# Kernel tuning notes

Measured on AMD Instinct MI355X. Metric: run time of the kernel, lower is better.

## Reference

```python
import jax, jax.numpy as jnp
import numpy as np

DIM = 1024
INTER = 1024
E = 8            # n_routed_experts
TOP_K = 2        # n_activated_experts
ROUTE_SCALE = 1.0
B, S = 2, 1024


def setup_inputs() -> dict:
    key = jax.random.key(0)
    ks = jax.random.split(key, 8)
    scale = 0.02
    x = jax.random.normal(ks[0], (B, S, DIM), dtype=jnp.float32)
    gate_w = jax.random.normal(ks[1], (DIM, E), dtype=jnp.float32) * scale
    w1 = jax.random.normal(ks[2], (E, DIM, INTER), dtype=jnp.float32) * scale
    w2 = jax.random.normal(ks[3], (E, INTER, DIM), dtype=jnp.float32) * scale
    w3 = jax.random.normal(ks[4], (E, DIM, INTER), dtype=jnp.float32) * scale
    sw1 = jax.random.normal(ks[5], (DIM, INTER), dtype=jnp.float32) * scale
    sw2 = jax.random.normal(ks[6], (INTER, DIM), dtype=jnp.float32) * scale
    sw3 = jax.random.normal(ks[7], (DIM, INTER), dtype=jnp.float32) * scale
    return {"x": x, "gate_w": gate_w, "w1": w1, "w2": w2, "w3": w3,
            "sw1": sw1, "sw2": sw2, "sw3": sw3}


def reference(x, gate_w, w1, w2, w3, sw1, sw2, sw3):
    b, s, d = x.shape
    xt = x.reshape(-1, d)                      # [T, D]
    T = xt.shape[0]

    # --- TokenChoiceTopKRouter (score_func='softmax') ---
    scores = jax.nn.softmax((xt @ gate_w).astype(jnp.float32), axis=-1)  # [T, E]
    top_scores, top_idx = jax.lax.top_k(scores, TOP_K)                   # [T, K]
    top_scores = top_scores * ROUTE_SCALE

    # Dense combine weights [T, E]: scatter top-k routing weights per token.
    cw = jnp.zeros((T, E), dtype=xt.dtype)
    cw = cw.at[jnp.arange(T)[:, None], top_idx].set(top_scores.astype(xt.dtype))

    # --- GroupedExperts: SwiGLU per routed expert ---
    h1 = jnp.einsum('td,edh->teh', xt, w1)     # [T, E, INTER]
    h3 = jnp.einsum('td,edh->teh', xt, w3)
    h = jax.nn.silu(h1) * h3
    expert_out = jnp.einsum('teh,ehd->ted', h, w2)   # [T, E, D]

    # Combine: weighted sum over activated experts (zero weight elsewhere).
    routed = jnp.einsum('ted,te->td', expert_out, cw)

    # --- Shared expert (runs on all tokens) ---
    shared = (jax.nn.silu(xt @ sw1) * (xt @ sw3)) @ sw2

    return (routed + shared).reshape(b, s, d)
```

## Files before the change

kernel.cpp:

```cpp
#include <hip/hip_runtime.h>
#include <hip/hip_bf16.h>
#include <cstdint>
#include <cstddef>

#define DIM   1024
#define INTER 1024
#define NT    2048

typedef __attribute__((ext_vector_type(4))) float  f32x4;
typedef __attribute__((ext_vector_type(8))) short  s16x8;
typedef __attribute__((ext_vector_type(8))) unsigned short u16x8;

#define WS_CNT    0u
#define WS_SLOT   256u
#define WS_ASSIGN 33024u
#define WS_WT     65792u
#define WS_WTS2   98560u
#define WS_XB     131584u
#define WS_H      4325888u
#define WS_W1T    16908800u
#define WS_W3T    33686016u
#define WS_W2T    50463232u
#define WS_SW1T   67240448u
#define WS_SW3T   69337600u
#define WS_SW2T   71434752u
#define WS_NEED   73531904u
#define WS_OBUF   WS_W1T

__device__ __forceinline__ unsigned short f2bf(float f) {
    unsigned int u = __float_as_uint(f);
    return (unsigned short)((u + 0x7fffu + ((u >> 16) & 1u)) >> 16);
}
__device__ __forceinline__ float bf2f(unsigned short v) {
    return __uint_as_float(((unsigned int)v) << 16);
}

__device__ __forceinline__ void cp16(const void* g, void* l) {
    __builtin_amdgcn_global_load_lds((const __attribute__((address_space(1))) void*)g,
                                     (__attribute__((address_space(3))) void*)l, 16, 0, 0);
}

__global__ __launch_bounds__(256) void kfat1(
    const float* __restrict__ x, const float* __restrict__ gw,
    const float* __restrict__ w1, const float* __restrict__ w3,
    const float* __restrict__ sw1, const float* __restrict__ sw3,
    unsigned short* __restrict__ w1t, unsigned short* __restrict__ w3t,
    unsigned short* __restrict__ sw1t, unsigned short* __restrict__ sw3t,
    int* __restrict__ assign, float2* __restrict__ wts2, unsigned short* __restrict__ xb)
{
    __shared__ __align__(16) char smem[65536];
    int bid = blockIdx.x;
    int tid = threadIdx.x;
    if (bid < 1152) {
        int slab = bid >> 6, t = bid & 63;
        int r0 = (t >> 3) * 128, c0 = (t & 7) * 128;
        const float* src; unsigned short* dst;
        if (slab < 8)        { src = w1 + (size_t)slab * DIM * INTER;       dst = w1t + (size_t)slab * DIM * INTER; }
        else if (slab < 16)  { src = w3 + (size_t)(slab - 8) * DIM * INTER; dst = w3t + (size_t)(slab - 8) * DIM * INTER; }
        else if (slab == 16) { src = sw1; dst = sw1t; }
        else                 { src = sw3; dst = sw3t; }

        char* buf0 = smem;
        char* buf1 = smem + 32768;
        int w = tid >> 6, l = tid & 63;
        size_t lanoff = (size_t)(l >> 5) * 4096 + (size_t)(l & 31) * 16;
        const char* gbase = (const char*)src + (size_t)r0 * 4096 + (size_t)c0 * 4;

        #pragma unroll
        for (int i = 0; i < 8; ++i)
            cp16(gbase + (size_t)(w * 16 + i * 2) * 4096 + lanoff, buf0 + (w * 16 + i * 2) * 512);
        #pragma unroll
        for (int i = 0; i < 8; ++i)
            cp16(gbase + (size_t)(64 + w * 16 + i * 2) * 4096 + lanoff, buf1 + (w * 16 + i * 2) * 512);

        asm volatile("s_waitcnt vmcnt(8)" ::: "memory");
        __builtin_amdgcn_sched_barrier(0);
        __builtin_amdgcn_s_barrier();
        __builtin_amdgcn_sched_barrier(0);
        {
            const float* ldsf = (const float*)buf0;
            #pragma unroll
            for (int i = 0; i < 4; ++i) {
                int f = w * 4 + i;
                int ntl = f >> 1, ktl = f & 1;
                u16x8 o;
                #pragma unroll
                for (int j = 0; j < 8; ++j)
                    o[j] = f2bf(ldsf[(ktl * 32 + (l >> 4) * 8 + j) * 128 + ntl * 16 + (l & 15)]);
                size_t off = ((size_t)((c0 >> 4) + ntl) * 32 + (r0 >> 5) + ktl) * 512 + l * 8;
                *(u16x8*)(dst + off) = o;
            }
        }
        asm volatile("s_waitcnt vmcnt(0)" ::: "memory");
        __builtin_amdgcn_sched_barrier(0);
        __builtin_amdgcn_s_barrier();
        __builtin_amdgcn_sched_barrier(0);
        {
            const float* ldsf = (const float*)buf1;
            #pragma unroll
            for (int i = 0; i < 4; ++i) {
                int f = w * 4 + i;
                int ntl = f >> 1, ktl = f & 1;
                u16x8 o;
                #pragma unroll
                for (int j = 0; j < 8; ++j)
                    o[j] = f2bf(ldsf[(ktl * 32 + (l >> 4) * 8 + j) * 128 + ntl * 16 + (l & 15)]);
                size_t off = ((size_t)((c0 >> 4) + ntl) * 32 + (r0 >> 5) + 2 + ktl) * 512 + l * 8;
                *(u16x8*)(dst + off) = o;
            }
        }
        return;
    }
    int wid = tid >> 6, lane = tid & 63;
    int t = (bid - 1152) * 4 + wid;
    const float* xrow = x + (size_t)t * DIM;

    float xr[16];
    float acc[8] = {0.f,0.f,0.f,0.f,0.f,0.f,0.f,0.f};
    #pragma unroll
    for (int j = 0; j < 16; ++j) {
        float xv = xrow[j * 64 + lane];
        xr[j] = xv;
        const f32x4* g = (const f32x4*)(gw + (size_t)(j * 64 + lane) * 8);
        f32x4 g0 = g[0], g1 = g[1];
        acc[0] += xv * g0[0]; acc[1] += xv * g0[1]; acc[2] += xv * g0[2]; acc[3] += xv * g0[3];
        acc[4] += xv * g1[0]; acc[5] += xv * g1[1]; acc[6] += xv * g1[2]; acc[7] += xv * g1[3];
    }
    #pragma unroll
    for (int j = 0; j < 16; ++j) xb[(size_t)t * DIM + j * 64 + lane] = f2bf(xr[j]);

    #pragma unroll
    for (int e = 0; e < 8; ++e) {
        float v = acc[e];
        v += __shfl_xor(v, 1);  v += __shfl_xor(v, 2);  v += __shfl_xor(v, 4);
        v += __shfl_xor(v, 8);  v += __shfl_xor(v, 16); v += __shfl_xor(v, 32);
        acc[e] = v;
    }
    float mx = acc[0];
    #pragma unroll
    for (int e = 1; e < 8; ++e) mx = fmaxf(mx, acc[e]);
    float p[8]; float se = 0.f;
    #pragma unroll
    for (int e = 0; e < 8; ++e) { p[e] = expf(acc[e] - mx); se += p[e]; }
    float inv = 1.0f / se;
    int i0 = 0; float b0 = p[0];
    #pragma unroll
    for (int e = 1; e < 8; ++e) if (p[e] > b0) { b0 = p[e]; i0 = e; }
    int i1 = -1; float b1 = -1.f;
    #pragma unroll
    for (int e = 0; e < 8; ++e) if (e != i0 && p[e] > b1) { b1 = p[e]; i1 = e; }
    if (lane == 0) {
        assign[t] = i0 | (i1 << 8);
        wts2[t] = make_float2(b0 * inv, b1 * inv);
    }
}

__global__ __launch_bounds__(256) void kscatter(const int* __restrict__ assign,
                                                const float2* __restrict__ wts2,
                                                int* __restrict__ cnt,
                                                int* __restrict__ slots,
                                                float* __restrict__ wts)
{
    __shared__ int h[8], pos[8];
    int tid = threadIdx.x, lane = tid & 63;
    if (tid < 8) h[tid] = 0;
    __syncthreads();

    for (int base = 0; base < NT; base += 256) {
        int a = assign[base + tid];
        int e0 = a & 255, e1 = (a >> 8) & 255;
        #pragma unroll
        for (int e = 0; e < 8; ++e) {
            unsigned long long m0 = __ballot(e0 == e);
            unsigned long long m1 = __ballot(e1 == e);
            if (lane == 0) {
                int c = __popcll(m0) + __popcll(m1);
                if (c) atomicAdd(&h[e], c);
            }
        }
    }
    __syncthreads();
    if (tid == 0) {
        int run = 0;
        #pragma unroll
        for (int e = 0; e < 8; ++e) {
            cnt[8 + e] = run; pos[e] = run;
            cnt[e] = h[e]; run += h[e];
        }
        cnt[16] = run;
    }
    __syncthreads();

    for (int base = 0; base < NT; base += 256) {
        int t = base + tid;
        int a = assign[t];
        float2 w = wts2[t];
        int e0 = a & 255, e1 = (a >> 8) & 255;
        unsigned long long lt = (1ull << lane) - 1ull;
        #pragma unroll
        for (int e = 0; e < 8; ++e) {
            unsigned long long m0 = __ballot(e0 == e);
            unsigned long long m1 = __ballot(e1 == e);
            int c = __popcll(m0) + __popcll(m1);
            int b = 0;
            if (lane == 0 && c) b = atomicAdd(&pos[e], c);
            b = __shfl(b, 0);
            if (e0 == e) { int r = __popcll(m0 & lt);                 slots[b + r] = t * 2;     wts[b + r] = w.x; }
            if (e1 == e) { int r = __popcll(m0) + __popcll(m1 & lt);  slots[b + r] = t * 2 + 1; wts[b + r] = w.y; }
        }
    }
}

__global__ __launch_bounds__(256) void kfat2(
    const unsigned short* __restrict__ xb,
    const unsigned short* __restrict__ w1t, const unsigned short* __restrict__ w3t,
    const unsigned short* __restrict__ sw1t, const unsigned short* __restrict__ sw3t,
    const int* __restrict__ cnt, const int* __restrict__ slots,
    unsigned short* __restrict__ hbuf,
    const float* __restrict__ w2, const float* __restrict__ sw2,
    unsigned short* __restrict__ w2t, unsigned short* __restrict__ sw2t)
{
    __shared__ __align__(16) char smem[34048];
    int z = blockIdx.z;
    int tid = threadIdx.x;
    if (z >= 9) {
        if (blockIdx.x >= 8) return;
        int slab = z - 9;
        const float* src; unsigned short* dst;
        if (slab < 8) { src = w2 + (size_t)slab * DIM * INTER; dst = w2t + (size_t)slab * DIM * INTER; }
        else          { src = sw2; dst = sw2t; }
        int r0 = blockIdx.y * 64, c0 = blockIdx.x * 128;

        int w = tid >> 6, l = tid & 63;
        size_t lanoff = (size_t)(l >> 5) * 4096 + (size_t)(l & 31) * 16;
        const char* gbase = (const char*)src + (size_t)r0 * 4096 + (size_t)c0 * 4;
        #pragma unroll
        for (int i = 0; i < 8; ++i)
            cp16(gbase + (size_t)(w * 16 + i * 2) * 4096 + lanoff, smem + (w * 16 + i * 2) * 512);
        asm volatile("s_waitcnt vmcnt(0)" ::: "memory");
        __builtin_amdgcn_sched_barrier(0);
        __builtin_amdgcn_s_barrier();
        __builtin_amdgcn_sched_barrier(0);
        const float* ldsf = (const float*)smem;
        #pragma unroll
        for (int i = 0; i < 4; ++i) {
            int f = w * 4 + i;
            int ntl = f >> 1, ktl = f & 1;
            u16x8 o;
            #pragma unroll
            for (int j = 0; j < 8; ++j)
                o[j] = f2bf(ldsf[(ktl * 32 + (l >> 4) * 8 + j) * 128 + ntl * 16 + (l & 15)]);
            size_t off = ((size_t)((c0 >> 4) + ntl) * 32 + (r0 >> 5) + ktl) * 512 + l * 8;
            *(u16x8*)(dst + off) = o;
        }
        return;
    }

    int e = z;
    int m0 = blockIdx.y * 128;
    int n0 = blockIdx.x * 64;
    int n_rows, lbase;
    if (e < 8) { n_rows = cnt[e]; lbase = cnt[8 + e]; } else { n_rows = NT; lbase = 0; }
    if (m0 >= n_rows) return;
    int rm = min(128, n_rows - m0);

    const unsigned short* b1p = (e < 8) ? (w1t + (size_t)e * DIM * INTER) : sw1t;
    const unsigned short* b3p = (e < 8) ? (w3t + (size_t)e * DIM * INTER) : sw3t;

    char* sA = smem;
    int* rowTok  = (int*)(smem + 32768);
    int* rowSlot = (int*)(smem + 33280);

    if (tid < 128) {
        int r = m0 + min(tid, rm - 1);
        int slot, tok;
        if (e < 8) { slot = slots[lbase + r]; tok = slot >> 1; }
        else       { tok = r; slot = 4096 + r; }
        rowTok[tid] = tok;
        rowSlot[tid] = slot;
    }
    __syncthreads();

    int wid = tid >> 6, lane = tid & 63;
    int wr = wid >> 1, wc = wid & 1;
    int swz_st = (((lane & 7) ^ (lane >> 3)) - (lane & 7)) * 16;

    const char* pA[4];
    #pragma unroll
    for (int q = 0; q < 4; ++q) {
        int row = (q * 4 + wid) * 8 + (lane >> 3);
        pA[q] = (const char*)(xb + (size_t)rowTok[row] * DIM) + (lane & 7) * 16 + swz_st;
    }
    const char* pB1[2]; const char* pB3[2];
    #pragma unroll
    for (int n = 0; n < 2; ++n) {
        int nt = (n0 >> 4) + wc * 2 + n;
        pB1[n] = (const char*)b1p + (size_t)nt * 32768 + lane * 16;
        pB3[n] = (const char*)b3p + (size_t)nt * 32768 + lane * 16;
    }

    int loA[2];
    #pragma unroll
    for (int ks = 0; ks < 2; ++ks) {
        int ch = ((ks * 4) + (lane >> 4)) ^ (lane & 7);
        loA[ks] = (wr * 64 + (lane & 15)) * 128 + ch * 16;
    }

    f32x4 acc1[4][2], acc3[4][2];
    #pragma unroll
    for (int m = 0; m < 4; ++m)
        #pragma unroll
        for (int n = 0; n < 2; ++n) { acc1[m][n] = (f32x4){0.f,0.f,0.f,0.f}; acc3[m][n] = (f32x4){0.f,0.f,0.f,0.f}; }

    s16x8 br1[2][2][2], br3[2][2][2];

    #pragma unroll
    for (int q = 0; q < 4; ++q) { cp16(pA[q], sA + (q * 4 + wid) * 1024); pA[q] += 128; }
    #pragma unroll
    for (int n = 0; n < 2; ++n)
        #pragma unroll
        for (int ks = 0; ks < 2; ++ks) {
            br1[0][n][ks] = *(const s16x8*)(pB1[n] + ks * 1024);
            br3[0][n][ks] = *(const s16x8*)(pB3[n] + ks * 1024);
        }

    for (int tt = 0; tt < 8; ++tt) {
        #pragma unroll
        for (int half = 0; half < 2; ++half) {
            if (half == 0 || tt < 7) {
                #pragma unroll
                for (int q = 0; q < 4; ++q) {
                    cp16(pA[q], sA + (half ^ 1) * 16384 + (q * 4 + wid) * 1024);
                    pA[q] += 128;
                }
                #pragma unroll
                for (int n = 0; n < 2; ++n)
                    #pragma unroll
                    for (int ks = 0; ks < 2; ++ks) {
                        br1[half ^ 1][n][ks] = *(const s16x8*)(pB1[n] + (half * 2 + 2 + ks) * 1024);
                        br3[half ^ 1][n][ks] = *(const s16x8*)(pB3[n] + (half * 2 + 2 + ks) * 1024);
                    }
                asm volatile("s_waitcnt vmcnt(12)" ::: "memory");
            } else {
                asm volatile("s_waitcnt vmcnt(0)" ::: "memory");
            }
            __builtin_amdgcn_sched_barrier(0);
            __builtin_amdgcn_s_barrier();
            __builtin_amdgcn_sched_barrier(0);

            #pragma unroll
            for (int ks = 0; ks < 2; ++ks) {
                s16x8 a[4];
                #pragma unroll
                for (int m = 0; m < 4; ++m)
                    a[m] = *(const s16x8*)(sA + half * 16384 + m * 2048 + loA[ks]);
                #pragma unroll
                for (int n = 0; n < 2; ++n) {
                    #pragma unroll
                    for (int m = 0; m < 4; ++m) {
                        acc1[m][n] = __builtin_amdgcn_mfma_f32_16x16x32_bf16(a[m], br1[half][n][ks], acc1[m][n], 0, 0, 0);
                        acc3[m][n] = __builtin_amdgcn_mfma_f32_16x16x32_bf16(a[m], br3[half][n][ks], acc3[m][n], 0, 0, 0);
                    }
                }
            }
            __builtin_amdgcn_sched_barrier(0);
            __builtin_amdgcn_s_barrier();
            __builtin_amdgcn_sched_barrier(0);
        }
        #pragma unroll
        for (int n = 0; n < 2; ++n) { pB1[n] += 4096; pB3[n] += 4096; }
    }

    #pragma unroll
    for (int m = 0; m < 4; ++m) {
        int rbase = wr * 64 + m * 16 + (lane >> 4) * 4;
        #pragma unroll
        for (int r = 0; r < 4; ++r) {
            int row = rbase + r;
            if (row < rm) {
                int hrow = rowSlot[row];
                #pragma unroll
                for (int n = 0; n < 2; ++n) {
                    float v1 = acc1[m][n][r], v3 = acc3[m][n][r];
                    float hv = (v1 / (1.0f + __expf(-v1))) * v3;
                    int col = n0 + wc * 32 + n * 16 + (lane & 15);
                    hbuf[(size_t)hrow * INTER + col] = f2bf(hv);
                }
            }
        }
    }
}

__global__ __launch_bounds__(256) void kgemm2(
    const unsigned short* __restrict__ hbuf,
    const unsigned short* __restrict__ w2t, const unsigned short* __restrict__ sw2t,
    const int* __restrict__ cnt, const int* __restrict__ slots,
    unsigned short* __restrict__ obuf)
{
    int e = blockIdx.z;
    int m0 = blockIdx.y * 128;
    int n0 = blockIdx.x * 64;
    int n_rows, lbase;
    if (e < 8) { n_rows = cnt[e]; lbase = cnt[8 + e]; } else { n_rows = NT; lbase = 0; }
    if (m0 >= n_rows) return;
    int rm = min(128, n_rows - m0);
    const unsigned short* bp = (e < 8) ? (w2t + (size_t)e * DIM * INTER) : sw2t;

    __shared__ __align__(16) char sA[2][16384];
    __shared__ int rowH[128];

    int tid = threadIdx.x;
    if (tid < 128) {
        int r = m0 + min(tid, rm - 1);
        rowH[tid] = (e < 8) ? slots[lbase + r] : (4096 + r);
    }
    __syncthreads();

    int wid = tid >> 6, lane = tid & 63;
    int wr = wid >> 1, wc = wid & 1;
    int swz_st = (((lane & 7) ^ (lane >> 3)) - (lane & 7)) * 16;

    const char* pA[4];
    #pragma unroll
    for (int q = 0; q < 4; ++q) {
        int row = (q * 4 + wid) * 8 + (lane >> 3);
        pA[q] = (const char*)(hbuf + (size_t)rowH[row] * INTER) + (lane & 7) * 16 + swz_st;
    }
    const char* pB[2];
    #pragma unroll
    for (int n = 0; n < 2; ++n) {
        int nt = (n0 >> 4) + wc * 2 + n;
        pB[n] = (const char*)bp + (size_t)nt * 32768 + lane * 16;
    }

    int loA[2];
    #pragma unroll
    for (int ks = 0; ks < 2; ++ks) {
        int ch = ((ks * 4) + (lane >> 4)) ^ (lane & 7);
        loA[ks] = (wr * 64 + (lane & 15)) * 128 + ch * 16;
    }

    f32x4 acc[4][2];
    #pragma unroll
    for (int m = 0; m < 4; ++m)
        #pragma unroll
        for (int n = 0; n < 2; ++n) acc[m][n] = (f32x4){0.f,0.f,0.f,0.f};

    s16x8 br[2][2][2];

    #pragma unroll
    for (int q = 0; q < 4; ++q) { cp16(pA[q], (char*)sA + (q * 4 + wid) * 1024); pA[q] += 128; }
    #pragma unroll
    for (int n = 0; n < 2; ++n)
        #pragma unroll
        for (int ks = 0; ks < 2; ++ks)
            br[0][n][ks] = *(const s16x8*)(pB[n] + ks * 1024);

    for (int tt = 0; tt < 8; ++tt) {
        #pragma unroll
        for (int half = 0; half < 2; ++half) {
            if (half == 0 || tt < 7) {
                #pragma unroll
                for (int q = 0; q < 4; ++q) {
                    cp16(pA[q], (char*)sA + (half ^ 1) * 16384 + (q * 4 + wid) * 1024);
                    pA[q] += 128;
                }
                #pragma unroll
                for (int n = 0; n < 2; ++n)
                    #pragma unroll
                    for (int ks = 0; ks < 2; ++ks)
                        br[half ^ 1][n][ks] = *(const s16x8*)(pB[n] + (half * 2 + 2 + ks) * 1024);
                asm volatile("s_waitcnt vmcnt(8)" ::: "memory");
            } else {
                asm volatile("s_waitcnt vmcnt(0)" ::: "memory");
            }
            __builtin_amdgcn_sched_barrier(0);
            __builtin_amdgcn_s_barrier();
            __builtin_amdgcn_sched_barrier(0);

            #pragma unroll
            for (int ks = 0; ks < 2; ++ks) {
                s16x8 a[4];
                #pragma unroll
                for (int m = 0; m < 4; ++m)
                    a[m] = *(const s16x8*)((const char*)sA + half * 16384 + m * 2048 + loA[ks]);
                #pragma unroll
                for (int n = 0; n < 2; ++n)
                    #pragma unroll
                    for (int m = 0; m < 4; ++m)
                        acc[m][n] = __builtin_amdgcn_mfma_f32_16x16x32_bf16(a[m], br[half][n][ks], acc[m][n], 0, 0, 0);
            }
            __builtin_amdgcn_sched_barrier(0);
            __builtin_amdgcn_s_barrier();
            __builtin_amdgcn_sched_barrier(0);
        }
        #pragma unroll
        for (int n = 0; n < 2; ++n) pB[n] += 4096;
    }

    #pragma unroll
    for (int m = 0; m < 4; ++m) {
        int rbase = wr * 64 + m * 16 + (lane >> 4) * 4;
        #pragma unroll
        for (int r = 0; r < 4; ++r) {
            int row = rbase + r;
            if (row < rm) {
                int orow = rowH[row];
                #pragma unroll
                for (int n = 0; n < 2; ++n) {
                    int col = n0 + wc * 32 + n * 16 + (lane & 15);
                    obuf[(size_t)orow * DIM + col] = f2bf(acc[m][n][r]);
                }
            }
        }
    }
}

__global__ __launch_bounds__(256) void kcombine(const unsigned short* __restrict__ obuf,
                                                const float2* __restrict__ wts2,
                                                float* __restrict__ out)
{
    int gid = blockIdx.x * 256 + threadIdx.x;
    int t = gid >> 7;
    int d0 = (gid & 127) * 8;
    float2 w = wts2[t];
    u16x8 r0 = *(const u16x8*)&obuf[(size_t)(2 * t)     * DIM + d0];
    u16x8 r1 = *(const u16x8*)&obuf[(size_t)(2 * t + 1) * DIM + d0];
    u16x8 rs = *(const u16x8*)&obuf[(size_t)(4096 + t)  * DIM + d0];
    f32x4 o0, o1;
    #pragma unroll
    for (int j = 0; j < 4; ++j) o0[j] = w.x * bf2f(r0[j]) + w.y * bf2f(r1[j]) + bf2f(rs[j]);
    #pragma unroll
    for (int j = 0; j < 4; ++j) o1[j] = w.x * bf2f(r0[4+j]) + w.y * bf2f(r1[4+j]) + bf2f(rs[4+j]);
    f32x4* dst = (f32x4*)&out[(size_t)t * DIM + d0];
    dst[0] = o0; dst[1] = o1;
}

extern "C" void kernel_launch(void* const* d_in, const int* in_sizes, int n_in,
                              void* d_out, int out_size, void* d_ws, size_t ws_size,
                              hipStream_t stream) {
    const float* x      = (const float*)d_in[0];
    const float* gate_w = (const float*)d_in[1];
    const float* w1     = (const float*)d_in[2];
    const float* w2     = (const float*)d_in[3];
    const float* w3     = (const float*)d_in[4];
    const float* sw1    = (const float*)d_in[5];
    const float* sw2    = (const float*)d_in[6];
    const float* sw3    = (const float*)d_in[7];
    float* out = (float*)d_out;

    if (ws_size < (size_t)WS_NEED) return;

    char* ws = (char*)d_ws;
    int*            cnt      = (int*)(ws + WS_CNT);
    int*            slots    = (int*)(ws + WS_SLOT);
    int*            assign   = (int*)(ws + WS_ASSIGN);
    float*          wts      = (float*)(ws + WS_WT);
    float2*         wts2     = (float2*)(ws + WS_WTS2);
    unsigned short* xb       = (unsigned short*)(ws + WS_XB);
    unsigned short* hbuf     = (unsigned short*)(ws + WS_H);
    unsigned short* w1t      = (unsigned short*)(ws + WS_W1T);
    unsigned short* w3t      = (unsigned short*)(ws + WS_W3T);
    unsigned short* w2t      = (unsigned short*)(ws + WS_W2T);
    unsigned short* sw1t     = (unsigned short*)(ws + WS_SW1T);
    unsigned short* sw3t     = (unsigned short*)(ws + WS_SW3T);
    unsigned short* sw2t     = (unsigned short*)(ws + WS_SW2T);
    unsigned short* obuf     = (unsigned short*)(ws + WS_OBUF);

    kfat1<<<dim3(1664), 256, 0, stream>>>(x, gate_w, w1, w3, sw1, sw3,
                                          w1t, w3t, sw1t, sw3t, assign, wts2, xb);
    kscatter<<<dim3(1), 256, 0, stream>>>(assign, wts2, cnt, slots, wts);
    kfat2<<<dim3(16, 16, 18), 256, 0, stream>>>(xb, w1t, w3t, sw1t, sw3t, cnt, slots, hbuf,
                                                w2, sw2, w2t, sw2t);
    kgemm2<<<dim3(16, 16, 9), 256, 0, stream>>>(hbuf, w2t, sw2t, cnt, slots, obuf);
    kcombine<<<dim3(1024), 256, 0, stream>>>(obuf, wts2, out);
}
```

Baseline: 133.4 us.

## Widen GEMM tiles to 128 columns with 512-thread blocks; split weight conversion finer

The grouped GEMM kernels (kfat2, kgemm2) now use 128x128 output tiles computed by 8 waves in 512-thread blocks instead of 128x64 tiles with 4 waves. Each wave now issues fewer A-tile async copies, and the vmcnt waits are adjusted to match. This halves the number of blocks and the redundant A-tile loads per output column, but lowers the block count available to fill the GPU. The weight-transpose/convert work in kfat1 is split into 64-row tiles without double buffering, doubling its block count and halving its LDS use. The w2 conversion inside kfat2 is also spread across all x-blocks, so none of them idle.

```diff
diff --git a/kernel.cpp b/kernel.cpp
--- a/kernel.cpp
+++ b/kernel.cpp
@@ -48,71 +48,44 @@
     unsigned short* __restrict__ sw1t, unsigned short* __restrict__ sw3t,
     int* __restrict__ assign, float2* __restrict__ wts2, unsigned short* __restrict__ xb)
 {
-    __shared__ __align__(16) char smem[65536];
+    __shared__ __align__(16) char smem[32768];
     int bid = blockIdx.x;
     int tid = threadIdx.x;
-    if (bid < 1152) {
-        int slab = bid >> 6, t = bid & 63;
-        int r0 = (t >> 3) * 128, c0 = (t & 7) * 128;
+    if (bid < 2304) {
+        int slab = bid >> 7, t = bid & 127;
+        int r0 = (t >> 3) * 64, c0 = (t & 7) * 128;
         const float* src; unsigned short* dst;
         if (slab < 8)        { src = w1 + (size_t)slab * DIM * INTER;       dst = w1t + (size_t)slab * DIM * INTER; }
         else if (slab < 16)  { src = w3 + (size_t)(slab - 8) * DIM * INTER; dst = w3t + (size_t)(slab - 8) * DIM * INTER; }
         else if (slab == 16) { src = sw1; dst = sw1t; }
         else                 { src = sw3; dst = sw3t; }
 
-        char* buf0 = smem;
-        char* buf1 = smem + 32768;
         int w = tid >> 6, l = tid & 63;
         size_t lanoff = (size_t)(l >> 5) * 4096 + (size_t)(l & 31) * 16;
         const char* gbase = (const char*)src + (size_t)r0 * 4096 + (size_t)c0 * 4;
-
         #pragma unroll
         for (int i = 0; i < 8; ++i)
-            cp16(gbase + (size_t)(w * 16 + i * 2) * 4096 + lanoff, buf0 + (w * 16 + i * 2) * 512);
-        #pragma unroll
-        for (int i = 0; i < 8; ++i)
-            cp16(gbase + (size_t)(64 + w * 16 + i * 2) * 4096 + lanoff, buf1 + (w * 16 + i * 2) * 512);
-
-        asm volatile("s_waitcnt vmcnt(8)" ::: "memory");
-        __builtin_amdgcn_sched_barrier(0);
-        __builtin_amdgcn_s_barrier();
-        __builtin_amdgcn_sched_barrier(0);
-        {
-            const float* ldsf = (const float*)buf0;
-            #pragma unroll
-            for (int i = 0; i < 4; ++i) {
-                int f = w * 4 + i;
-                int ntl = f >> 1, ktl = f & 1;
-                u16x8 o;
-                #pragma unroll
-                for (int j = 0; j < 8; ++j)
-                    o[j] = f2bf(ldsf[(ktl * 32 + (l >> 4) * 8 + j) * 128 + ntl * 16 + (l & 15)]);
-                size_t off = ((size_t)((c0 >> 4) + ntl) * 32 + (r0 >> 5) + ktl) * 512 + l * 8;
-                *(u16x8*)(dst + off) = o;
-            }
-        }
+            cp16(gbase + (size_t)(w * 16 + i * 2) * 4096 + lanoff, smem + (w * 16 + i * 2) * 512);
         asm volatile("s_waitcnt vmcnt(0)" ::: "memory");
         __builtin_amdgcn_sched_barrier(0);
         __builtin_amdgcn_s_barrier();
         __builtin_amdgcn_sched_barrier(0);
-        {
-            const float* ldsf = (const float*)buf1;
+        const float* ldsf = (const float*)smem;
+        #pragma unroll
+        for (int i = 0; i < 4; ++i) {
+            int f = w * 4 + i;
+            int ntl = f >> 1, ktl = f & 1;
+            u16x8 o;
             #pragma unroll
-            for (int i = 0; i < 4; ++i) {
-                int f = w * 4 + i;
-                int ntl = f >> 1, ktl = f & 1;
-                u16x8 o;
-                #pragma unroll
-                for (int j = 0; j < 8; ++j)
-                    o[j] = f2bf(ldsf[(ktl * 32 + (l >> 4) * 8 + j) * 128 + ntl * 16 + (l & 15)]);
-                size_t off = ((size_t)((c0 >> 4) + ntl) * 32 + (r0 >> 5) + 2 + ktl) * 512 + l * 8;
-                *(u16x8*)(dst + off) = o;
-            }
+            for (int j = 0; j < 8; ++j)
+                o[j] = f2bf(ldsf[(ktl * 32 + (l >> 4) * 8 + j) * 128 + ntl * 16 + (l & 15)]);
+            size_t off = ((size_t)((c0 >> 4) + ntl) * 32 + (r0 >> 5) + ktl) * 512 + l * 8;
+            *(u16x8*)(dst + off) = o;
         }
         return;
     }
     int wid = tid >> 6, lane = tid & 63;
-    int t = (bid - 1152) * 4 + wid;
+    int t = (bid - 2304) * 4 + wid;
     const float* xrow = x + (size_t)t * DIM;
 
     float xr[16];
@@ -211,7 +184,7 @@
     }
 }
 
-__global__ __launch_bounds__(256) void kfat2(
+__global__ __launch_bounds__(512) void kfat2(
     const unsigned short* __restrict__ xb,
     const unsigned short* __restrict__ w1t, const unsigned short* __restrict__ w3t,
     const unsigned short* __restrict__ sw1t, const unsigned short* __restrict__ sw3t,
@@ -220,11 +193,10 @@
     const float* __restrict__ w2, const float* __restrict__ sw2,
     unsigned short* __restrict__ w2t, unsigned short* __restrict__ sw2t)
 {
-    __shared__ __align__(16) char smem[34048];
+    __shared__ __align__(16) char smem[33792];
     int z = blockIdx.z;
     int tid = threadIdx.x;
     if (z >= 9) {
-        if (blockIdx.x >= 8) return;
         int slab = z - 9;
         const float* src; unsigned short* dst;
         if (slab < 8) { src = w2 + (size_t)slab * DIM * INTER; dst = w2t + (size_t)slab * DIM * INTER; }
@@ -235,16 +207,16 @@
         size_t lanoff = (size_t)(l >> 5) * 4096 + (size_t)(l & 31) * 16;
         const char* gbase = (const char*)src + (size_t)r0 * 4096 + (size_t)c0 * 4;
         #pragma unroll
-        for (int i = 0; i < 8; ++i)
-            cp16(gbase + (size_t)(w * 16 + i * 2) * 4096 + lanoff, smem + (w * 16 + i * 2) * 512);
+        for (int i = 0; i < 4; ++i)
+            cp16(gbase + (size_t)(w * 8 + i * 2) * 4096 + lanoff, smem + (w * 8 + i * 2) * 512);
         asm volatile("s_waitcnt vmcnt(0)" ::: "memory");
         __builtin_amdgcn_sched_barrier(0);
         __builtin_amdgcn_s_barrier();
         __builtin_amdgcn_sched_barrier(0);
         const float* ldsf = (const float*)smem;
         #pragma unroll
-        for (int i = 0; i < 4; ++i) {
-            int f = w * 4 + i;
+        for (int i = 0; i < 2; ++i) {
+            int f = w * 2 + i;
             int ntl = f >> 1, ktl = f & 1;
             u16x8 o;
             #pragma unroll
@@ -258,7 +230,7 @@
 
     int e = z;
     int m0 = blockIdx.y * 128;
-    int n0 = blockIdx.x * 64;
+    int n0 = blockIdx.x * 128;
     int n_rows, lbase;
     if (e < 8) { n_rows = cnt[e]; lbase = cnt[8 + e]; } else { n_rows = NT; lbase = 0; }
     if (m0 >= n_rows) return;
@@ -282,13 +254,13 @@
     __syncthreads();
 
     int wid = tid >> 6, lane = tid & 63;
-    int wr = wid >> 1, wc = wid & 1;
+    int wr = wid >> 2, wc = wid & 3;
     int swz_st = (((lane & 7) ^ (lane >> 3)) - (lane & 7)) * 16;
 
-    const char* pA[4];
-    #pragma unroll
-    for (int q = 0; q < 4; ++q) {
-        int row = (q * 4 + wid) * 8 + (lane >> 3);
+    const char* pA[2];
+    #pragma unroll
+    for (int q = 0; q < 2; ++q) {
+        int row = (q * 8 + wid) * 8 + (lane >> 3);
         pA[q] = (const char*)(xb + (size_t)rowTok[row] * DIM) + (lane & 7) * 16 + swz_st;
     }
     const char* pB1[2]; const char* pB3[2];
@@ -315,7 +287,7 @@
     s16x8 br1[2][2][2], br3[2][2][2];
 
     #pragma unroll
-    for (int q = 0; q < 4; ++q) { cp16(pA[q], sA + (q * 4 + wid) * 1024); pA[q] += 128; }
+    for (int q = 0; q < 2; ++q) { cp16(pA[q], sA + (q * 8 + wid) * 1024); pA[q] += 128; }
     #pragma unroll
     for (int n = 0; n < 2; ++n)
         #pragma unroll
@@ -329,8 +301,8 @@
         for (int half = 0; half < 2; ++half) {
             if (half == 0 || tt < 7) {
                 #pragma unroll
-                for (int q = 0; q < 4; ++q) {
-                    cp16(pA[q], sA + (half ^ 1) * 16384 + (q * 4 + wid) * 1024);
+                for (int q = 0; q < 2; ++q) {
+                    cp16(pA[q], sA + (half ^ 1) * 16384 + (q * 8 + wid) * 1024);
                     pA[q] += 128;
                 }
                 #pragma unroll
@@ -340,7 +312,7 @@
                         br1[half ^ 1][n][ks] = *(const s16x8*)(pB1[n] + (half * 2 + 2 + ks) * 1024);
                         br3[half ^ 1][n][ks] = *(const s16x8*)(pB3[n] + (half * 2 + 2 + ks) * 1024);
                     }
-                asm volatile("s_waitcnt vmcnt(12)" ::: "memory");
+                asm volatile("s_waitcnt vmcnt(10)" ::: "memory");
             } else {
                 asm volatile("s_waitcnt vmcnt(0)" ::: "memory");
             }
@@ -391,7 +363,7 @@
     }
 }
 
-__global__ __launch_bounds__(256) void kgemm2(
+__global__ __launch_bounds__(512) void kgemm2(
     const unsigned short* __restrict__ hbuf,
     const unsigned short* __restrict__ w2t, const unsigned short* __restrict__ sw2t,
     const int* __restrict__ cnt, const int* __restrict__ slots,
@@ -399,7 +371,7 @@
 {
     int e = blockIdx.z;
     int m0 = blockIdx.y * 128;
-    int n0 = blockIdx.x * 64;
+    int n0 = blockIdx.x * 128;
     int n_rows, lbase;
     if (e < 8) { n_rows = cnt[e]; lbase = cnt[8 + e]; } else { n_rows = NT; lbase = 0; }
     if (m0 >= n_rows) return;
@@ -417,13 +389,13 @@
     __syncthreads();
 
     int wid = tid >> 6, lane = tid & 63;
-    int wr = wid >> 1, wc = wid & 1;
+    int wr = wid >> 2, wc = wid & 3;
     int swz_st = (((lane & 7) ^ (lane >> 3)) - (lane & 7)) * 16;
 
-    const char* pA[4];
-    #pragma unroll
-    for (int q = 0; q < 4; ++q) {
-        int row = (q * 4 + wid) * 8 + (lane >> 3);
+    const char* pA[2];
+    #pragma unroll
+    for (int q = 0; q < 2; ++q) {
+        int row = (q * 8 + wid) * 8 + (lane >> 3);
         pA[q] = (const char*)(hbuf + (size_t)rowH[row] * INTER) + (lane & 7) * 16 + swz_st;
     }
     const char* pB[2];
@@ -449,7 +421,7 @@
     s16x8 br[2][2][2];
 
     #pragma unroll
-    for (int q = 0; q < 4; ++q) { cp16(pA[q], (char*)sA + (q * 4 + wid) * 1024); pA[q] += 128; }
+    for (int q = 0; q < 2; ++q) { cp16(pA[q], (char*)sA + (q * 8 + wid) * 1024); pA[q] += 128; }
     #pragma unroll
     for (int n = 0; n < 2; ++n)
         #pragma unroll
@@ -461,8 +433,8 @@
         for (int half = 0; half < 2; ++half) {
             if (half == 0 || tt < 7) {
                 #pragma unroll
-                for (int q = 0; q < 4; ++q) {
-                    cp16(pA[q], (char*)sA + (half ^ 1) * 16384 + (q * 4 + wid) * 1024);
+                for (int q = 0; q < 2; ++q) {
+                    cp16(pA[q], (char*)sA + (half ^ 1) * 16384 + (q * 8 + wid) * 1024);
                     pA[q] += 128;
                 }
                 #pragma unroll
@@ -470,7 +442,7 @@
                     #pragma unroll
                     for (int ks = 0; ks < 2; ++ks)
                         br[half ^ 1][n][ks] = *(const s16x8*)(pB[n] + (half * 2 + 2 + ks) * 1024);
-                asm volatile("s_waitcnt vmcnt(8)" ::: "memory");
+                asm volatile("s_waitcnt vmcnt(6)" ::: "memory");
             } else {
                 asm volatile("s_waitcnt vmcnt(0)" ::: "memory");
             }
@@ -567,11 +539,11 @@
     unsigned short* sw2t     = (unsigned short*)(ws + WS_SW2T);
     unsigned short* obuf     = (unsigned short*)(ws + WS_OBUF);
 
-    kfat1<<<dim3(1664), 256, 0, stream>>>(x, gate_w, w1, w3, sw1, sw3,
+    kfat1<<<dim3(2816), 256, 0, stream>>>(x, gate_w, w1, w3, sw1, sw3,
                                           w1t, w3t, sw1t, sw3t, assign, wts2, xb);
     kscatter<<<dim3(1), 256, 0, stream>>>(assign, wts2, cnt, slots, wts);
-    kfat2<<<dim3(16, 16, 18), 256, 0, stream>>>(xb, w1t, w3t, sw1t, sw3t, cnt, slots, hbuf,
-                                                w2, sw2, w2t, sw2t);
-    kgemm2<<<dim3(16, 16, 9), 256, 0, stream>>>(hbuf, w2t, sw2t, cnt, slots, obuf);
+    kfat2<<<dim3(8, 16, 18), 512, 0, stream>>>(xb, w1t, w3t, sw1t, sw3t, cnt, slots, hbuf,
+                                               w2, sw2, w2t, sw2t);
+    kgemm2<<<dim3(8, 16, 9), 512, 0, stream>>>(hbuf, w2t, sw2t, cnt, slots, obuf);
     kcombine<<<dim3(1024), 256, 0, stream>>>(obuf, wts2, out);
 }
```

New measurement: 145.4 us. 9.1% more time.

## Split weight-convert tiles and move B-register prefetch after MFMA compute

Applied to the files above, without the earlier changes.

The weight conversion blocks in kfat1 now each handle a 64x128 tile with a single 32KB LDS buffer instead of two 64-row halves in 64KB. This doubles the block count and cuts LDS per block, which should raise occupancy. In both GEMM kernels the main loop is peeled so that B-fragment register loads for the next stage are issued after the current MFMAs rather than before the wait. That gives global loads more time in flight, but it adds duplicated epilogue code and extra barriers.

```diff
diff --git a/kernel.cpp b/kernel.cpp
--- a/kernel.cpp
+++ b/kernel.cpp
@@ -48,71 +48,44 @@
     unsigned short* __restrict__ sw1t, unsigned short* __restrict__ sw3t,
     int* __restrict__ assign, float2* __restrict__ wts2, unsigned short* __restrict__ xb)
 {
-    __shared__ __align__(16) char smem[65536];
+    __shared__ __align__(16) char smem[32768];
     int bid = blockIdx.x;
     int tid = threadIdx.x;
-    if (bid < 1152) {
-        int slab = bid >> 6, t = bid & 63;
-        int r0 = (t >> 3) * 128, c0 = (t & 7) * 128;
+    if (bid < 2304) {
+        int slab = bid >> 7, t = bid & 127;
+        int r0 = (t >> 3) * 64, c0 = (t & 7) * 128;
         const float* src; unsigned short* dst;
         if (slab < 8)        { src = w1 + (size_t)slab * DIM * INTER;       dst = w1t + (size_t)slab * DIM * INTER; }
         else if (slab < 16)  { src = w3 + (size_t)(slab - 8) * DIM * INTER; dst = w3t + (size_t)(slab - 8) * DIM * INTER; }
         else if (slab == 16) { src = sw1; dst = sw1t; }
         else                 { src = sw3; dst = sw3t; }
 
-        char* buf0 = smem;
-        char* buf1 = smem + 32768;
         int w = tid >> 6, l = tid & 63;
         size_t lanoff = (size_t)(l >> 5) * 4096 + (size_t)(l & 31) * 16;
         const char* gbase = (const char*)src + (size_t)r0 * 4096 + (size_t)c0 * 4;
-
         #pragma unroll
         for (int i = 0; i < 8; ++i)
-            cp16(gbase + (size_t)(w * 16 + i * 2) * 4096 + lanoff, buf0 + (w * 16 + i * 2) * 512);
-        #pragma unroll
-        for (int i = 0; i < 8; ++i)
-            cp16(gbase + (size_t)(64 + w * 16 + i * 2) * 4096 + lanoff, buf1 + (w * 16 + i * 2) * 512);
-
-        asm volatile("s_waitcnt vmcnt(8)" ::: "memory");
-        __builtin_amdgcn_sched_barrier(0);
-        __builtin_amdgcn_s_barrier();
-        __builtin_amdgcn_sched_barrier(0);
-        {
-            const float* ldsf = (const float*)buf0;
-            #pragma unroll
-            for (int i = 0; i < 4; ++i) {
-                int f = w * 4 + i;
-                int ntl = f >> 1, ktl = f & 1;
-                u16x8 o;
-                #pragma unroll
-                for (int j = 0; j < 8; ++j)
-                    o[j] = f2bf(ldsf[(ktl * 32 + (l >> 4) * 8 + j) * 128 + ntl * 16 + (l & 15)]);
-                size_t off = ((size_t)((c0 >> 4) + ntl) * 32 + (r0 >> 5) + ktl) * 512 + l * 8;
-                *(u16x8*)(dst + off) = o;
-            }
-        }
+            cp16(gbase + (size_t)(w * 16 + i * 2) * 4096 + lanoff, smem + (w * 16 + i * 2) * 512);
         asm volatile("s_waitcnt vmcnt(0)" ::: "memory");
         __builtin_amdgcn_sched_barrier(0);
         __builtin_amdgcn_s_barrier();
         __builtin_amdgcn_sched_barrier(0);
-        {
-            const float* ldsf = (const float*)buf1;
-            #pragma unroll
-            for (int i = 0; i < 4; ++i) {
-                int f = w * 4 + i;
-                int ntl = f >> 1, ktl = f & 1;
-                u16x8 o;
-                #pragma unroll
-                for (int j = 0; j < 8; ++j)
-                    o[j] = f2bf(ldsf[(ktl * 32 + (l >> 4) * 8 + j) * 128 + ntl * 16 + (l & 15)]);
-                size_t off = ((size_t)((c0 >> 4) + ntl) * 32 + (r0 >> 5) + 2 + ktl) * 512 + l * 8;
-                *(u16x8*)(dst + off) = o;
-            }
+        const float* ldsf = (const float*)smem;
+        #pragma unroll
+        for (int i = 0; i < 4; ++i) {
+            int f = w * 4 + i;
+            int ntl = f >> 1, ktl = f & 1;
+            u16x8 o;
+            #pragma unroll
+            for (int j = 0; j < 8; ++j)
+                o[j] = f2bf(ldsf[(ktl * 32 + (l >> 4) * 8 + j) * 128 + ntl * 16 + (l & 15)]);
+            size_t off = ((size_t)((c0 >> 4) + ntl) * 32 + (r0 >> 5) + ktl) * 512 + l * 8;
+            *(u16x8*)(dst + off) = o;
         }
         return;
     }
     int wid = tid >> 6, lane = tid & 63;
-    int t = (bid - 1152) * 4 + wid;
+    int t = (bid - 2304) * 4 + wid;
     const float* xrow = x + (size_t)t * DIM;
 
     float xr[16];
@@ -323,27 +296,23 @@
             br1[0][n][ks] = *(const s16x8*)(pB1[n] + ks * 1024);
             br3[0][n][ks] = *(const s16x8*)(pB3[n] + ks * 1024);
         }
-
-    for (int tt = 0; tt < 8; ++tt) {
+    #pragma unroll
+    for (int n = 0; n < 2; ++n)
+        #pragma unroll
+        for (int ks = 0; ks < 2; ++ks) {
+            br1[1][n][ks] = *(const s16x8*)(pB1[n] + (2 + ks) * 1024);
+            br3[1][n][ks] = *(const s16x8*)(pB3[n] + (2 + ks) * 1024);
+        }
+
+    for (int tt = 0; tt < 7; ++tt) {
         #pragma unroll
         for (int half = 0; half < 2; ++half) {
-            if (half == 0 || tt < 7) {
-                #pragma unroll
-                for (int q = 0; q < 4; ++q) {
-                    cp16(pA[q], sA + (half ^ 1) * 16384 + (q * 4 + wid) * 1024);
-                    pA[q] += 128;
-                }
-                #pragma unroll
-                for (int n = 0; n < 2; ++n)
-                    #pragma unroll
-                    for (int ks = 0; ks < 2; ++ks) {
-                        br1[half ^ 1][n][ks] = *(const s16x8*)(pB1[n] + (half * 2 + 2 + ks) * 1024);
-                        br3[half ^ 1][n][ks] = *(const s16x8*)(pB3[n] + (half * 2 + 2 + ks) * 1024);
-                    }
-                asm volatile("s_waitcnt vmcnt(12)" ::: "memory");
-            } else {
-                asm volatile("s_waitcnt vmcnt(0)" ::: "memory");
-            }
+            #pragma unroll
+            for (int q = 0; q < 4; ++q) {
+                cp16(pA[q], sA + (half ^ 1) * 16384 + (q * 4 + wid) * 1024);
+                pA[q] += 128;
+            }
+            asm volatile("s_waitcnt vmcnt(12)" ::: "memory");
             __builtin_amdgcn_sched_barrier(0);
             __builtin_amdgcn_s_barrier();
             __builtin_amdgcn_sched_barrier(0);
@@ -363,12 +332,60 @@
                     }
                 }
             }
+            #pragma unroll
+            for (int n = 0; n < 2; ++n)
+                #pragma unroll
+                for (int ks = 0; ks < 2; ++ks) {
+                    br1[half][n][ks] = *(const s16x8*)(pB1[n] + (half * 2 + 4 + ks) * 1024);
+                    br3[half][n][ks] = *(const s16x8*)(pB3[n] + (half * 2 + 4 + ks) * 1024);
+                }
             __builtin_amdgcn_sched_barrier(0);
             __builtin_amdgcn_s_barrier();
             __builtin_amdgcn_sched_barrier(0);
         }
         #pragma unroll
         for (int n = 0; n < 2; ++n) { pB1[n] += 4096; pB3[n] += 4096; }
+    }
+    #pragma unroll
+    for (int q = 0; q < 4; ++q) cp16(pA[q], sA + 16384 + (q * 4 + wid) * 1024);
+    asm volatile("s_waitcnt vmcnt(12)" ::: "memory");
+    __builtin_amdgcn_sched_barrier(0);
+    __builtin_amdgcn_s_barrier();
+    __builtin_amdgcn_sched_barrier(0);
+    #pragma unroll
+    for (int ks = 0; ks < 2; ++ks) {
+        s16x8 a[4];
+        #pragma unroll
+        for (int m = 0; m < 4; ++m)
+            a[m] = *(const s16x8*)(sA + m * 2048 + loA[ks]);
+        #pragma unroll
+        for (int n = 0; n < 2; ++n)
+            #pragma unroll
+            for (int m = 0; m < 4; ++m) {
+                acc1[m][n] = __builtin_amdgcn_mfma_f32_16x16x32_bf16(a[m], br1[0][n][ks], acc1[m][n], 0, 0, 0);
+                acc3[m][n] = __builtin_amdgcn_mfma_f32_16x16x32_bf16(a[m], br3[0][n][ks], acc3[m][n], 0, 0, 0);
+            }
+    }
+    __builtin_amdgcn_sched_barrier(0);
+    __builtin_amdgcn_s_barrier();
+    __builtin_amdgcn_sched_barrier(0);
+    asm volatile("s_waitcnt vmcnt(0)" ::: "memory");
+    __builtin_amdgcn_sched_barrier(0);
+    __builtin_amdgcn_s_barrier();
+    __builtin_amdgcn_sched_barrier(0);
+    #pragma unroll
+    for (int ks = 0; ks < 2; ++ks) {
+        s16x8 a[4];
+        #pragma unroll
+        for (int m = 0; m < 4; ++m)
+            a[m] = *(const s16x8*)(sA + 16384 + m * 2048 + loA[ks]);
+        #pragma unroll
+        for (int n = 0; n < 2; ++n)
+            #pragma unroll
+            for (int m = 0; m < 4; ++m) {
+                acc1[m][n] = __builtin_amdgcn_mfma_f32_16x16x32_bf16(a[m], br1[1][n][ks], acc1[m][n], 0, 0, 0);
+                acc3[m][n] = __builtin_amdgcn_mfma_f32_16x16x32_bf16(a[m], br3[1][n][ks], acc3[m][n], 0, 0, 0);
+            }
     }
 
     #pragma unroll
@@ -455,25 +472,21 @@
         #pragma unroll
         for (int ks = 0; ks < 2; ++ks)
             br[0][n][ks] = *(const s16x8*)(pB[n] + ks * 1024);
-
-    for (int tt = 0; tt < 8; ++tt) {
+    #pragma unroll
+    for (int n = 0; n < 2; ++n)
+        #pragma unroll
+        for (int ks = 0; ks < 2; ++ks)
+            br[1][n][ks] = *(const s16x8*)(pB[n] + (2 + ks) * 1024);
+
+    for (int tt = 0; tt < 7; ++tt) {
         #pragma unroll
         for (int half = 0; half < 2; ++half) {
-            if (half == 0 || tt < 7) {
-                #pragma unroll
-                for (int q = 0; q < 4; ++q) {
-                    cp16(pA[q], (char*)sA + (half ^ 1) * 16384 + (q * 4 + wid) * 1024);
-                    pA[q] += 128;
-                }
-                #pragma unroll
-                for (int n = 0; n < 2; ++n)
-                    #pragma unroll
-                    for (int ks = 0; ks < 2; ++ks)
-                        br[half ^ 1][n][ks] = *(const s16x8*)(pB[n] + (half * 2 + 2 + ks) * 1024);
-                asm volatile("s_waitcnt vmcnt(8)" ::: "memory");
-            } else {
-                asm volatile("s_waitcnt vmcnt(0)" ::: "memory");
-            }
+            #pragma unroll
+            for (int q = 0; q < 4; ++q) {
+                cp16(pA[q], (char*)sA + (half ^ 1) * 16384 + (q * 4 + wid) * 1024);
+                pA[q] += 128;
+            }
+            asm volatile("s_waitcnt vmcnt(8)" ::: "memory");
             __builtin_amdgcn_sched_barrier(0);
             __builtin_amdgcn_s_barrier();
             __builtin_amdgcn_sched_barrier(0);
@@ -490,12 +503,54 @@
                     for (int m = 0; m < 4; ++m)
                         acc[m][n] = __builtin_amdgcn_mfma_f32_16x16x32_bf16(a[m], br[half][n][ks], acc[m][n], 0, 0, 0);
             }
+            #pragma unroll
+            for (int n = 0; n < 2; ++n)
+                #pragma unroll
+                for (int ks = 0; ks < 2; ++ks)
+                    br[half][n][ks] = *(const s16x8*)(pB[n] + (half * 2 + 4 + ks) * 1024);
             __builtin_amdgcn_sched_barrier(0);
             __builtin_amdgcn_s_barrier();
             __builtin_amdgcn_sched_barrier(0);
         }
         #pragma unroll
         for (int n = 0; n < 2; ++n) pB[n] += 4096;
+    }
+    #pragma unroll
+    for (int q = 0; q < 4; ++q) cp16(pA[q], (char*)sA + 16384 + (q * 4 + wid) * 1024);
+    asm volatile("s_waitcnt vmcnt(8)" ::: "memory");
+    __builtin_amdgcn_sched_barrier(0);
+    __builtin_amdgcn_s_barrier();
+    __builtin_amdgcn_sched_barrier(0);
+    #pragma unroll
+    for (int ks = 0; ks < 2; ++ks) {
+        s16x8 a[4];
+        #pragma unroll
+        for (int m = 0; m < 4; ++m)
+            a[m] = *(const s16x8*)((const char*)sA + m * 2048 + loA[ks]);
+        #pragma unroll
+        for (int n = 0; n < 2; ++n)
+            #pragma unroll
+            for (int m = 0; m < 4; ++m)
+                acc[m][n] = __builtin_amdgcn_mfma_f32_16x16x32_bf16(a[m], br[0][n][ks], acc[m][n], 0, 0, 0);
+    }
+    __builtin_amdgcn_sched_barrier(0);
+    __builtin_amdgcn_s_barrier();
+    __builtin_amdgcn_sched_barrier(0);
+    asm volatile("s_waitcnt vmcnt(0)" ::: "memory");
+    __builtin_amdgcn_sched_barrier(0);
+    __builtin_amdgcn_s_barrier();
+    __builtin_amdgcn_sched_barrier(0);
+    #pragma unroll
+    for (int ks = 0; ks < 2; ++ks) {
+        s16x8 a[4];
+        #pragma unroll
+        for (int m = 0; m < 4; ++m)
+            a[m] = *(const s16x8*)((const char*)sA + 16384 + m * 2048 + loA[ks]);
+        #pragma unroll
+        for (int n = 0; n < 2; ++n)
+            #pragma unroll
+            for (int m = 0; m < 4; ++m)
+                acc[m][n] = __builtin_amdgcn_mfma_f32_16x16x32_bf16(a[m], br[1][n][ks], acc[m][n], 0, 0, 0);
     }
 
     #pragma unroll
@@ -567,7 +622,7 @@
     unsigned short* sw2t     = (unsigned short*)(ws + WS_SW2T);
     unsigned short* obuf     = (unsigned short*)(ws + WS_OBUF);
 
-    kfat1<<<dim3(1664), 256, 0, stream>>>(x, gate_w, w1, w3, sw1, sw3,
+    kfat1<<<dim3(2816), 256, 0, stream>>>(x, gate_w, w1, w3, sw1, sw3,
                                           w1t, w3t, sw1t, sw3t, assign, wts2, xb);
     kscatter<<<dim3(1), 256, 0, stream>>>(assign, wts2, cnt, slots, wts);
     kfat2<<<dim3(16, 16, 18), 256, 0, stream>>>(xb, w1t, w3t, sw1t, sw3t, cnt, slots, hbuf,
```

After: 127.5 us. -4.4%, faster.
